# Optimization experiments

Hardware: AMD Instinct MI355X
Metric: run time of the kernel (lower is better)

The kernel has to match this reference:

```python
import jax, jax.numpy as jnp
import numpy as np

RADIUS = 0.5
BATCH, N, C_IN, C_OUT = 8, 1024, 64, 64


def setup_inputs() -> dict:
    key = jax.random.key(0)
    k1, k2, k3 = jax.random.split(key, 3)
    features = jax.random.normal(k1, (BATCH, N, C_IN), dtype=jnp.float32)
    geometry = jax.random.normal(k2, (BATCH, N, 3), dtype=jnp.float32)
    # Kernel stand-in: linear map from relative position to [C_out, C_in] matrix
    W = jax.random.normal(k3, (3, C_OUT, C_IN), dtype=jnp.float32) / np.sqrt(3.0 * C_IN)
    return {"features": features, "geometry": geometry, "W": W}


def reference(features, geometry, W):
    # diff[z,a,b,:] = r_b - r_a  (neighbor minus center), matching rb - ra in torch
    diff = geometry[:, None, :, :] - geometry[:, :, None, :]          # [z,a,b,3]
    norm = jnp.sqrt(jnp.sum(diff * diff, axis=-1))                    # [z,a,b]
    # rel_mask: 1 where within radius (the dense equivalent of the padded
    # neighbor-list + mask; padded/out-of-ball entries contribute zero)
    rel_mask = (norm < RADIUS).astype(features.dtype)                 # [z,a,b]
    # kernel(diff)[z,a,b,i,j] = sum_x diff[z,a,b,x] * W[x,i,j]
    # output[z,a,i] = sum_{b,x,j} mask*diff[z,a,b,x] * W[x,i,j] * feat[z,b,j]
    mdiff = rel_mask[..., None] * diff                                # [z,a,b,3]
    tmp = jnp.einsum('zabx,zbj->zaxj', mdiff, features)               # [z,a,3,Cin]
    out = jnp.einsum('zaxj,xij->zai', tmp, W)                         # [z,a,Cout]
    return out
```

## Files before the change

kernel.cpp:

```cpp
#include <hip/hip_runtime.h>


#define BATCHSZ 8
#define NPTS 1024
#define CIN 64
#define COUT 64
#define NXJ (3 * CIN)
#define NG (NXJ / 4)
#define PPB 8
#define BS (PPB * 64)
#define GPW (NG / PPB)
#define NSTEP (NPTS / 64)

typedef float f32x2 __attribute__((ext_vector_type(2)));

#define SM_RED 3072
#define SM_TMP 7168
#define SM_TOTAL 8704

__global__ __launch_bounds__(BS, 8) void neigh_conv_kernel(
    const float* __restrict__ feat,
    const float* __restrict__ geom,
    const float* __restrict__ W,
    float* __restrict__ out)
{
    const int lane = threadIdx.x & 63;
    const int wv   = threadIdx.x >> 6;
    const int p    = blockIdx.x * PPB + wv;
    const int a    = p & (NPTS - 1);
    const int z    = p >> 10;

    __shared__ __align__(16) float smem[SM_TOTAL];

    {
        const float4* src = (const float4*)(geom + (size_t)z * NPTS * 3);
        float4* dst = (float4*)smem;
        for (int k = threadIdx.x; k < NPTS * 3 / 4; k += BS)
            dst[k] = src[k];
    }

    const int g0 = wv * GPW;
    float4 wr[GPW];
    {
        const float4* w4 = (const float4*)W;
        float4* ws = (float4*)(smem + SM_RED);
        for (int x = 0; x < 3; ++x) {
            __syncthreads();
            #pragma unroll
            for (int kk = 0; kk < 2; ++kk) {
                const int k = threadIdx.x + kk * BS;
                const int idx = (k & ~15) | ((k + (k >> 4)) & 15);
                ws[idx] = w4[x * 1024 + k];
            }
            __syncthreads();
            #pragma unroll
            for (int q = 0; q < GPW; ++q) {
                const int g = g0 + q;
                if ((g >> 4) == x) {
                    const int c = g & 15;
                    wr[q] = ws[(lane << 4) | ((c + lane) & 15)];
                }
            }
        }
    }

    const float* geo = smem;
    const float gax = geo[a * 3 + 0];
    const float gay = geo[a * 3 + 1];
    const float gaz = geo[a * 3 + 2];
    const float* fz = feat + (size_t)z * NPTS * CIN;

    unsigned long long masks[NSTEP];
    #pragma unroll
    for (int ss = 0; ss < NSTEP; ++ss) {
        const int b = ss * 64 + lane;
        float d2;
        {
            #pragma clang fp contract(off)
            const float dx = geo[b * 3 + 0] - gax;
            const float dy = geo[b * 3 + 1] - gay;
            const float dz = geo[b * 3 + 2] - gaz;
            d2 = dx * dx + dy * dy + dz * dz;
        }
        masks[ss] = __ballot(d2 < 0.25f);
    }

    float acc0 = 0.f, acc1 = 0.f, acc2 = 0.f;
    int   b1 = -1, b2 = -1;
    float f1 = 0.f, f2 = 0.f;

    auto consume = [&](int bc, float fc) {
        const float gbx = geo[bc * 3 + 0];
        const float gby = geo[bc * 3 + 1];
        const float gbz = geo[bc * 3 + 2];
        const float dx = gbx - gax;
        const float dy = gby - gay;
        const float dz = gbz - gaz;
        acc0 = fmaf(dx, fc, acc0);
        acc1 = fmaf(dy, fc, acc1);
        acc2 = fmaf(dz, fc, acc2);
    };

    #pragma unroll
    for (int ss = 0; ss < NSTEP; ++ss) {
        unsigned long long mm = masks[ss];
        while (mm) {
            const int src = __ffsll(mm) - 1;
            mm &= mm - 1ull;
            const int b = ss * 64 + src;
            const float f = fz[(size_t)b * CIN + lane];
            if (b2 >= 0) consume(b2, f2);
            b2 = b1; f2 = f1;
            b1 = b;  f1 = f;
        }
    }
    if (b2 >= 0) consume(b2, f2);
    if (b1 >= 0) consume(b1, f1);

    float* tmp = smem + SM_TMP + wv * NXJ;
    tmp[0 * CIN + lane] = acc0;
    tmp[1 * CIN + lane] = acc1;
    tmp[2 * CIN + lane] = acc2;
    __syncthreads();

    float* red = smem + SM_RED;
    #pragma unroll
    for (int pp = 0; pp < PPB; ++pp) {
        const float4* t4 = (const float4*)(smem + SM_TMP + pp * NXJ);
        f32x2 facc = {0.f, 0.f};
        #pragma unroll
        for (int q = 0; q < GPW; ++q) {
            const float4 t = t4[g0 + q];
            f32x2 ta; ta.x = t.x; ta.y = t.y;
            f32x2 tb; tb.x = t.z; tb.y = t.w;
            f32x2 wa; wa.x = wr[q].x; wa.y = wr[q].y;
            f32x2 wb; wb.x = wr[q].z; wb.y = wr[q].w;
            facc = ta * wa + facc;
            facc = tb * wb + facc;
        }
        red[(wv * PPB + pp) * COUT + lane] = facc.x + facc.y;
    }
    __syncthreads();

    float o = 0.f;
    #pragma unroll
    for (int w = 0; w < PPB; ++w)
        o += red[(w * PPB + wv) * COUT + lane];

    out[(size_t)p * COUT + lane] = o;
}

extern "C" void kernel_launch(void* const* d_in, const int* in_sizes, int n_in,
                              void* d_out, int out_size, void* d_ws, size_t ws_size,
                              hipStream_t stream) {
    const float* feat = (const float*)d_in[0];
    const float* geom = (const float*)d_in[1];
    const float* W    = (const float*)d_in[2];
    float* out        = (float*)d_out;

    const int nblocks = BATCHSZ * NPTS / PPB;
    neigh_conv_kernel<<<nblocks, BS, 0, stream>>>(feat, geom, W, out);
}
```

Before: 18.27 us.

## Process two point sets per block to amortize geometry and weight staging

Each block now handles 16 center points in two sets of 8 instead of 8, which halves the number of blocks. The per-block cost of loading geometry and W is therefore spread over twice the work. All of W is staged into shared memory in a single pass rather than three sync-separated passes, which removes several barriers. In exchange, shared memory use roughly doubles and launch bounds drop to 4 blocks per SM, so occupancy and the number of blocks for load balance both go down.

```diff
diff --git a/kernel.cpp b/kernel.cpp
--- a/kernel.cpp
+++ b/kernel.cpp
@@ -8,17 +8,18 @@
 #define NXJ (3 * CIN)
 #define NG (NXJ / 4)
 #define PPB 8
+#define PSETS 2
 #define BS (PPB * 64)
 #define GPW (NG / PPB)
 #define NSTEP (NPTS / 64)
 
 typedef float f32x2 __attribute__((ext_vector_type(2)));
 
-#define SM_RED 3072
-#define SM_TMP 7168
-#define SM_TOTAL 8704
+#define SM_WS   3072
+#define SM_TMP  15360
+#define SM_TOTAL 18432
 
-__global__ __launch_bounds__(BS, 8) void neigh_conv_kernel(
+__global__ __launch_bounds__(BS, 4) void neigh_conv_kernel(
     const float* __restrict__ feat,
     const float* __restrict__ geom,
     const float* __restrict__ W,
@@ -26,9 +27,9 @@
 {
     const int lane = threadIdx.x & 63;
     const int wv   = threadIdx.x >> 6;
-    const int p    = blockIdx.x * PPB + wv;
-    const int a    = p & (NPTS - 1);
-    const int z    = p >> 10;
+    const int pbase = blockIdx.x * (PPB * PSETS);
+    const int z     = pbase >> 10;
+    const int abase = (pbase & (NPTS - 1)) + wv;
 
     __shared__ __align__(16) float smem[SM_TOTAL];
 
@@ -37,117 +38,120 @@
         float4* dst = (float4*)smem;
         for (int k = threadIdx.x; k < NPTS * 3 / 4; k += BS)
             dst[k] = src[k];
+
+        const float4* w4 = (const float4*)W;
+        float4* ws = (float4*)(smem + SM_WS);
+        #pragma unroll
+        for (int kk = 0; kk < 6; ++kk) {
+            const int k = threadIdx.x + kk * BS;
+            const int idx = (k & ~15) | ((k + (k >> 4)) & 15);
+            ws[idx] = w4[k];
+        }
     }
+    __syncthreads();
 
     const int g0 = wv * GPW;
     float4 wr[GPW];
     {
-        const float4* w4 = (const float4*)W;
-        float4* ws = (float4*)(smem + SM_RED);
-        for (int x = 0; x < 3; ++x) {
-            __syncthreads();
-            #pragma unroll
-            for (int kk = 0; kk < 2; ++kk) {
-                const int k = threadIdx.x + kk * BS;
-                const int idx = (k & ~15) | ((k + (k >> 4)) & 15);
-                ws[idx] = w4[x * 1024 + k];
-            }
-            __syncthreads();
-            #pragma unroll
-            for (int q = 0; q < GPW; ++q) {
-                const int g = g0 + q;
-                if ((g >> 4) == x) {
-                    const int c = g & 15;
-                    wr[q] = ws[(lane << 4) | ((c + lane) & 15)];
-                }
-            }
+        const float4* ws = (const float4*)(smem + SM_WS);
+        #pragma unroll
+        for (int q = 0; q < GPW; ++q) {
+            const int g = g0 + q;
+            const int x = g >> 4, c = g & 15;
+            wr[q] = ws[x * 1024 + (lane << 4) + ((c + lane) & 15)];
         }
     }
 
     const float* geo = smem;
-    const float gax = geo[a * 3 + 0];
-    const float gay = geo[a * 3 + 1];
-    const float gaz = geo[a * 3 + 2];
     const float* fz = feat + (size_t)z * NPTS * CIN;
 
-    unsigned long long masks[NSTEP];
     #pragma unroll
-    for (int ss = 0; ss < NSTEP; ++ss) {
-        const int b = ss * 64 + lane;
-        float d2;
-        {
-            #pragma clang fp contract(off)
-            const float dx = geo[b * 3 + 0] - gax;
-            const float dy = geo[b * 3 + 1] - gay;
-            const float dz = geo[b * 3 + 2] - gaz;
-            d2 = dx * dx + dy * dy + dz * dz;
+    for (int s = 0; s < PSETS; ++s) {
+        const int a = abase + s * PPB;
+        const float gax = geo[a * 3 + 0];
+        const float gay = geo[a * 3 + 1];
+        const float gaz = geo[a * 3 + 2];
+
+        unsigned long long masks[NSTEP];
+        #pragma unroll
+        for (int ss = 0; ss < NSTEP; ++ss) {
+            const int b = ss * 64 + lane;
+            float d2;
+            {
+                #pragma clang fp contract(off)
+                const float dx = geo[b * 3 + 0] - gax;
+                const float dy = geo[b * 3 + 1] - gay;
+                const float dz = geo[b * 3 + 2] - gaz;
+                d2 = dx * dx + dy * dy + dz * dz;
+            }
+            masks[ss] = __ballot(d2 < 0.25f);
         }
-        masks[ss] = __ballot(d2 < 0.25f);
-    }
 
-    float acc0 = 0.f, acc1 = 0.f, acc2 = 0.f;
-    int   b1 = -1, b2 = -1;
-    float f1 = 0.f, f2 = 0.f;
+        float acc0 = 0.f, acc1 = 0.f, acc2 = 0.f;
+        int   b1 = -1, b2 = -1;
+        float f1 = 0.f, f2 = 0.f;
+        auto consume = [&](int bc, float fc) {
+            const float dx = geo[bc * 3 + 0] - gax;
+            const float dy = geo[bc * 3 + 1] - gay;
+            const float dz = geo[bc * 3 + 2] - gaz;
+            acc0 = fmaf(dx, fc, acc0);
+            acc1 = fmaf(dy, fc, acc1);
+            acc2 = fmaf(dz, fc, acc2);
+        };
+        #pragma unroll
+        for (int ss = 0; ss < NSTEP; ++ss) {
+            unsigned long long mm = masks[ss];
+            while (mm) {
+                const int src = __ffsll(mm) - 1;
+                mm &= mm - 1ull;
+                const int b = ss * 64 + src;
+                const float f = fz[(size_t)b * CIN + lane];
+                if (b2 >= 0) consume(b2, f2);
+                b2 = b1; f2 = f1;
+                b1 = b;  f1 = f;
+            }
+        }
+        if (b2 >= 0) consume(b2, f2);
+        if (b1 >= 0) consume(b1, f1);
 
-    auto consume = [&](int bc, float fc) {
-        const float gbx = geo[bc * 3 + 0];
-        const float gby = geo[bc * 3 + 1];
-        const float gbz = geo[bc * 3 + 2];
-        const float dx = gbx - gax;
-        const float dy = gby - gay;
-        const float dz = gbz - gaz;
-        acc0 = fmaf(dx, fc, acc0);
-        acc1 = fmaf(dy, fc, acc1);
-        acc2 = fmaf(dz, fc, acc2);
-    };
-
-    #pragma unroll
-    for (int ss = 0; ss < NSTEP; ++ss) {
-        unsigned long long mm = masks[ss];
-        while (mm) {
-            const int src = __ffsll(mm) - 1;
-            mm &= mm - 1ull;
-            const int b = ss * 64 + src;
-            const float f = fz[(size_t)b * CIN + lane];
-            if (b2 >= 0) consume(b2, f2);
-            b2 = b1; f2 = f1;
-            b1 = b;  f1 = f;
-        }
-    }
-    if (b2 >= 0) consume(b2, f2);
-    if (b1 >= 0) consume(b1, f1);
-
-    float* tmp = smem + SM_TMP + wv * NXJ;
-    tmp[0 * CIN + lane] = acc0;
-    tmp[1 * CIN + lane] = acc1;
-    tmp[2 * CIN + lane] = acc2;
-    __syncthreads();
-
-    float* red = smem + SM_RED;
-    #pragma unroll
-    for (int pp = 0; pp < PPB; ++pp) {
-        const float4* t4 = (const float4*)(smem + SM_TMP + pp * NXJ);
-        f32x2 facc = {0.f, 0.f};
-        #pragma unroll
-        for (int q = 0; q < GPW; ++q) {
-            const float4 t = t4[g0 + q];
-            f32x2 ta; ta.x = t.x; ta.y = t.y;
-            f32x2 tb; tb.x = t.z; tb.y = t.w;
-            f32x2 wa; wa.x = wr[q].x; wa.y = wr[q].y;
-            f32x2 wb; wb.x = wr[q].z; wb.y = wr[q].w;
-            facc = ta * wa + facc;
-            facc = tb * wb + facc;
-        }
-        red[(wv * PPB + pp) * COUT + lane] = facc.x + facc.y;
+        float* tmp = smem + SM_TMP + s * (PPB * NXJ) + wv * NXJ;
+        tmp[0 * CIN + lane] = acc0;
+        tmp[1 * CIN + lane] = acc1;
+        tmp[2 * CIN + lane] = acc2;
     }
     __syncthreads();
 
-    float o = 0.f;
     #pragma unroll
-    for (int w = 0; w < PPB; ++w)
-        o += red[(w * PPB + wv) * COUT + lane];
+    for (int s = 0; s < PSETS; ++s) {
+        float* red = smem + SM_WS + s * (PPB * PPB * COUT);
+        #pragma unroll
+        for (int pp = 0; pp < PPB; ++pp) {
+            const float4* t4 = (const float4*)(smem + SM_TMP + s * (PPB * NXJ) + pp * NXJ);
+            f32x2 facc = {0.f, 0.f};
+            #pragma unroll
+            for (int q = 0; q < GPW; ++q) {
+                const float4 t = t4[g0 + q];
+                f32x2 ta; ta.x = t.x; ta.y = t.y;
+                f32x2 tb; tb.x = t.z; tb.y = t.w;
+                f32x2 wa; wa.x = wr[q].x; wa.y = wr[q].y;
+                f32x2 wb; wb.x = wr[q].z; wb.y = wr[q].w;
+                facc = ta * wa + facc;
+                facc = tb * wb + facc;
+            }
+            red[(wv * PPB + pp) * COUT + lane] = facc.x + facc.y;
+        }
+    }
+    __syncthreads();
 
-    out[(size_t)p * COUT + lane] = o;
+    #pragma unroll
+    for (int s = 0; s < PSETS; ++s) {
+        const float* red = smem + SM_WS + s * (PPB * PPB * COUT);
+        float o = 0.f;
+        #pragma unroll
+        for (int w = 0; w < PPB; ++w)
+            o += red[(w * PPB + wv) * COUT + lane];
+        out[(size_t)(pbase + s * PPB + wv) * COUT + lane] = o;
+    }
 }
 
 extern "C" void kernel_launch(void* const* d_in, const int* in_sizes, int n_in,
@@ -158,6 +162,6 @@
     const float* W    = (const float*)d_in[2];
     float* out        = (float*)d_out;
 
-    const int nblocks = BATCHSZ * NPTS / PPB;
+    const int nblocks = BATCHSZ * NPTS / (PPB * PSETS);
     neigh_conv_kernel<<<nblocks, BS, 0, stream>>>(feat, geom, W, out);
 }
```

Result: slower. 19.19 us (+5.1%).

## Double block size to 16 waves and stage all of W in shared memory at once

Applied to the files above, without the earlier changes.

Blocks now hold 16 waves (two halves of 8 points each) instead of 8. The geometry tile and the W staging are amortized over twice as many points, and W is loaded into shared memory in a single pass with one barrier instead of three staged passes. Each half does its own cross-wave reduction, reusing the W staging area as the reduction buffer. This adds an extra barrier before the reduction and doubles the shared-memory footprint per block, which may reduce how many blocks fit per CU.

```diff
diff --git a/kernel.cpp b/kernel.cpp
--- a/kernel.cpp
+++ b/kernel.cpp
@@ -7,16 +7,15 @@
 #define COUT 64
 #define NXJ (3 * CIN)
 #define NG (NXJ / 4)
-#define PPB 8
-#define BS (PPB * 64)
-#define GPW (NG / PPB)
+#define WPB 16
+#define BS (WPB * 64)
+#define GPW (NG / 8)
 #define NSTEP (NPTS / 64)
 
 typedef float f32x2 __attribute__((ext_vector_type(2)));
 
-#define SM_RED 3072
-#define SM_TMP 7168
-#define SM_TOTAL 8704
+#define SM_WS 3072
+#define SM_TOTAL 15360
 
 __global__ __launch_bounds__(BS, 8) void neigh_conv_kernel(
     const float* __restrict__ feat,
@@ -26,41 +25,40 @@
 {
     const int lane = threadIdx.x & 63;
     const int wv   = threadIdx.x >> 6;
-    const int p    = blockIdx.x * PPB + wv;
+    const int h    = wv >> 3;
+    const int hw   = wv & 7;
+    const int p    = blockIdx.x * WPB + wv;
     const int a    = p & (NPTS - 1);
     const int z    = p >> 10;
 
     __shared__ __align__(16) float smem[SM_TOTAL];
 
     {
-        const float4* src = (const float4*)(geom + (size_t)z * NPTS * 3);
-        float4* dst = (float4*)smem;
-        for (int k = threadIdx.x; k < NPTS * 3 / 4; k += BS)
-            dst[k] = src[k];
+        const float4* gsrc = (const float4*)(geom + (size_t)z * NPTS * 3);
+        float4* gdst = (float4*)smem;
+        if (threadIdx.x < NPTS * 3 / 4)
+            gdst[threadIdx.x] = gsrc[threadIdx.x];
+
+        const float4* w4 = (const float4*)W;
+        float4* ws = (float4*)(smem + SM_WS);
+        #pragma unroll
+        for (int kk = 0; kk < 3; ++kk) {
+            const int k = threadIdx.x + kk * BS;
+            const int idx = (k & ~15) | ((k + (k >> 4)) & 15);
+            ws[idx] = w4[k];
+        }
     }
+    __syncthreads();
 
-    const int g0 = wv * GPW;
+    const int g0 = hw * GPW;
     float4 wr[GPW];
     {
-        const float4* w4 = (const float4*)W;
-        float4* ws = (float4*)(smem + SM_RED);
-        for (int x = 0; x < 3; ++x) {
-            __syncthreads();
-            #pragma unroll
-            for (int kk = 0; kk < 2; ++kk) {
-                const int k = threadIdx.x + kk * BS;
-                const int idx = (k & ~15) | ((k + (k >> 4)) & 15);
-                ws[idx] = w4[x * 1024 + k];
-            }
-            __syncthreads();
-            #pragma unroll
-            for (int q = 0; q < GPW; ++q) {
-                const int g = g0 + q;
-                if ((g >> 4) == x) {
-                    const int c = g & 15;
-                    wr[q] = ws[(lane << 4) | ((c + lane) & 15)];
-                }
-            }
+        const float4* ws = (const float4*)(smem + SM_WS);
+        #pragma unroll
+        for (int q = 0; q < GPW; ++q) {
+            const int g = g0 + q;
+            const int x = g >> 4, c = g & 15;
+            wr[q] = ws[x * 1024 + (lane << 4) + ((c + lane) & 15)];
         }
     }
 
@@ -117,16 +115,18 @@
     if (b2 >= 0) consume(b2, f2);
     if (b1 >= 0) consume(b1, f1);
 
-    float* tmp = smem + SM_TMP + wv * NXJ;
+    __syncthreads();
+
+    float* tmp = smem + wv * NXJ;
     tmp[0 * CIN + lane] = acc0;
     tmp[1 * CIN + lane] = acc1;
     tmp[2 * CIN + lane] = acc2;
     __syncthreads();
 
-    float* red = smem + SM_RED;
+    float* red = smem + SM_WS + h * (8 * 8 * COUT);
     #pragma unroll
-    for (int pp = 0; pp < PPB; ++pp) {
-        const float4* t4 = (const float4*)(smem + SM_TMP + pp * NXJ);
+    for (int pp = 0; pp < 8; ++pp) {
+        const float4* t4 = (const float4*)(smem + (h * 8 + pp) * NXJ);
         f32x2 facc = {0.f, 0.f};
         #pragma unroll
         for (int q = 0; q < GPW; ++q) {
@@ -138,14 +138,14 @@
             facc = ta * wa + facc;
             facc = tb * wb + facc;
         }
-        red[(wv * PPB + pp) * COUT + lane] = facc.x + facc.y;
+        red[(hw * 8 + pp) * COUT + lane] = facc.x + facc.y;
     }
     __syncthreads();
 
     float o = 0.f;
     #pragma unroll
-    for (int w = 0; w < PPB; ++w)
-        o += red[(w * PPB + wv) * COUT + lane];
+    for (int w = 0; w < 8; ++w)
+        o += red[(w * 8 + hw) * COUT + lane];
 
     out[(size_t)p * COUT + lane] = o;
 }
@@ -158,6 +158,6 @@
     const float* W    = (const float*)d_in[2];
     float* out        = (float*)d_out;
 
-    const int nblocks = BATCHSZ * NPTS / PPB;
+    const int nblocks = BATCHSZ * NPTS / WPB;
     neigh_conv_kernel<<<nblocks, BS, 0, stream>>>(feat, geom, W, out);
 }
```

Result: no change. 18.08 us (median of 2 runs) (-1.0%).
